# Performance work log

Hardware: AMD Instinct MI355X
Metric: run time of the kernel (lower is better)

The kernel has to match this reference:

```python
import jax, jax.numpy as jnp
import numpy as np

B, N, D, NH = 16, 512, 4096, 16
DK = D // NH  # 256; note N must equal 2*DK for the bias broadcast to be valid


def setup_inputs() -> dict:
    key = jax.random.key(0)
    ks = jax.random.split(key, 7)
    s = 1.0 / np.sqrt(D).astype(np.float32)
    return {
        "x": jax.random.normal(ks[0], (B, N, D), dtype=jnp.float32),
        "Augementation_embedding": jax.random.normal(ks[1], (B, N, D), dtype=jnp.float32),
        "Wq": jax.random.normal(ks[2], (D, D), dtype=jnp.float32) * s,
        "Wk": jax.random.normal(ks[3], (D, D), dtype=jnp.float32) * s,
        "Wv": jax.random.normal(ks[4], (D, D), dtype=jnp.float32) * s,
        "Wp": jax.random.normal(ks[5], (2 * D, D), dtype=jnp.float32) * s,
        "bp": jax.random.normal(ks[6], (2 * D,), dtype=jnp.float32) * 0.01,
    }


def reference(x, Augementation_embedding, Wq, Wk, Wv, Wp, bp):
    b, n, d = x.shape
    nh, dk = NH, DK
    scale = 1.0 / np.sqrt(dk)
    # torch nn.Linear computes x @ W.T
    q = (x @ Wq.T).reshape(b, n, nh, dk).transpose(0, 2, 1, 3)  # (b,nh,n,dk)
    k = (x @ Wk.T).reshape(b, n, nh, dk).transpose(0, 2, 1, 3)
    v = (x @ Wv.T).reshape(b, n, nh, dk).transpose(0, 2, 1, 3)
    # additive learned bias: (b,nh,n,2*dk) == (b,nh,n,n) since n == 2*dk
    ep = (Augementation_embedding @ Wp.T + bp).reshape(b, n, nh, 2 * dk).transpose(0, 2, 1, 3)
    dist = jnp.einsum("bhqd,bhkd->bhqk", q, k) * scale + ep  # (b,nh,n,n)
    dist = jax.nn.softmax(dist, axis=-1)
    att = jnp.einsum("bhqk,bhkd->bhqd", dist, v)  # (b,nh,n,dk)
    return att.transpose(0, 2, 1, 3).reshape(b, n, d)
```

## Files before the change

### kernel.cpp

```cpp
#include <hip/hip_runtime.h>
#include <hip/hip_bf16.h>

typedef __attribute__((ext_vector_type(4))) float f32x4;
typedef __attribute__((ext_vector_type(8))) short s16x8;
typedef __attribute__((ext_vector_type(4))) short s16x4;
typedef __attribute__((ext_vector_type(8))) unsigned short u16x8;
typedef __attribute__((ext_vector_type(4))) unsigned short u16x4;
typedef __attribute__((ext_vector_type(4))) float fv4;

#define DEV static __device__ __forceinline__

DEV unsigned short f2bf(float f) {
  union { float f; unsigned u; } v; v.f = f;
  return (unsigned short)((v.u + 0x7fffu + ((v.u >> 16) & 1u)) >> 16);
}
DEV float bf2f(unsigned short u) {
  union { unsigned u; float f; } v; v.u = ((unsigned)u) << 16; return v.f;
}

typedef const __attribute__((address_space(1))) void* gas_t;
typedef __attribute__((address_space(3))) void* las_t;
DEV void load_lds16(const void* g, void* l) {
  __builtin_amdgcn_global_load_lds((gas_t)g, (las_t)l, 16, 0, 0);
}

__global__ __launch_bounds__(256) void cvt_kernel(const float* __restrict__ in,
                                                  unsigned short* __restrict__ out,
                                                  int n4) {
  int i = blockIdx.x * 256 + threadIdx.x;
  int stride = gridDim.x * 256;
  for (; i < n4; i += stride) {
    fv4 v = *(const fv4*)(in + (size_t)i * 4);
    u16x4 o;
    o[0] = f2bf(v[0]); o[1] = f2bf(v[1]); o[2] = f2bf(v[2]); o[3] = f2bf(v[3]);
    *(u16x4*)(out + (size_t)i * 4) = o;
  }
}

template<int EPI>
__global__ __launch_bounds__(256, 2) void gemm128(const unsigned short* __restrict__ A,
                                                  const unsigned short* __restrict__ B,
                                                  unsigned short* __restrict__ C,
                                                  const float* __restrict__ bias,
                                                  int N, int K, int bxsh) {
  __shared__ unsigned short lds[3][12288];
  const int t = threadIdx.x;
  const int lane = t & 63;
  const int w = t >> 6;
  const int wr = w >> 1;
  const int wc = w & 1;
  const int r0 = lane & 15;
  const int g = lane >> 4;

  const int bid = blockIdx.x;
  const int bx = bid & ((1 << bxsh) - 1);
  const int by = bid >> bxsh;
  const long brow = (long)by * 128;
  const long bcol = (long)bx * 256;

  const int srow = t >> 2;
  const int scol = ((t & 3) ^ ((t >> 3) & 3)) * 8;
  const unsigned short* As = A + (brow + srow) * (long)K + scol;
  const unsigned short* Bs = B + (bcol + srow) * (long)K + scol;
  const int dst = t * 8;

#define STG(sl, kt)                                                  \
  do {                                                               \
    const long c0_ = (long)(kt) << 5;                                \
    load_lds16(As + c0_,                   &lds[sl][dst]);           \
    load_lds16(As + 64 * (long)K + c0_,    &lds[sl][2048 + dst]);    \
    load_lds16(Bs + c0_,                   &lds[sl][4096 + dst]);    \
    load_lds16(Bs + 64 * (long)K + c0_,    &lds[sl][6144 + dst]);    \
    load_lds16(Bs + 128 * (long)K + c0_,   &lds[sl][8192 + dst]);    \
    load_lds16(Bs + 192 * (long)K + c0_,   &lds[sl][10240 + dst]);   \
  } while (0)
#define SBAR __builtin_amdgcn_sched_barrier(0)

  f32x4 acc[4][8] = {};
  const int NT = K >> 5;

  const int cswz = (g ^ ((r0 >> 1) & 3)) * 8;
  const int arow = wr * 64 + r0;
  const int brw = wc * 128 + r0;

  if (bid & 1) __builtin_amdgcn_s_sleep(8);

  STG(0, 0);
  STG(1, 1);
  asm volatile("s_waitcnt vmcnt(6)" ::: "memory");
  __builtin_amdgcn_s_barrier();
  SBAR;

  int sl = 0;
  for (int kt = 0; kt < NT; ++kt) {
    int sl2 = sl + 2; if (sl2 >= 3) sl2 -= 3;
    if (kt + 2 < NT) STG(sl2, kt + 2);
    const unsigned short* Lp = &lds[sl][0];
    s16x8 AF[4], BF[8];
#pragma unroll
    for (int m = 0; m < 4; ++m)
      AF[m] = *(const s16x8*)&Lp[(arow + m * 16) * 32 + cswz];
#pragma unroll
    for (int n = 0; n < 8; ++n)
      BF[n] = *(const s16x8*)&Lp[4096 + (brw + n * 16) * 32 + cswz];
    SBAR;
    __builtin_amdgcn_s_setprio(1);
#pragma unroll
    for (int m = 0; m < 4; ++m)
#pragma unroll
      for (int n = 0; n < 8; ++n)
        acc[m][n] = __builtin_amdgcn_mfma_f32_16x16x32_bf16(AF[m], BF[n], acc[m][n], 0, 0, 0);
    __builtin_amdgcn_s_setprio(0);
    SBAR;
    if (kt + 2 < NT) asm volatile("s_waitcnt vmcnt(6)" ::: "memory");
    else             asm volatile("s_waitcnt vmcnt(0)" ::: "memory");
    __builtin_amdgcn_s_barrier();
    SBAR;
    sl = (sl == 2) ? 0 : sl + 1;
  }
#undef SBAR
#undef STG

  const int g4 = g * 4;
#pragma unroll
  for (int m = 0; m < 4; ++m) {
#pragma unroll
    for (int n = 0; n < 8; ++n) {
      f32x4 v = acc[m][n];
      long col = bcol + wc * 128 + n * 16 + r0;
#pragma unroll
      for (int r = 0; r < 4; ++r) {
        long row = brow + wr * 64 + m * 16 + g4 + r;
        float val = v[r];
        if (EPI == 1) val += bias[col];
        if (EPI == 2) {
          long addr = ((col >> 9) << 21) + (row << 9) + (col & 511);
          C[addr] = f2bf(val);
        } else {
          C[row * (long)N + col] = f2bf(val);
        }
      }
    }
  }
}

__global__ __launch_bounds__(512, 2) void attn_kernel(const unsigned short* __restrict__ Q,
                                                      const unsigned short* __restrict__ K,
                                                      const unsigned short* __restrict__ V,
                                                      const unsigned short* __restrict__ EP,
                                                      float* __restrict__ out) {
  __shared__ unsigned short lds[256 * 136];
  const int t = threadIdx.x;
  const int lane = t & 63;
  const int w = t >> 6;
  const int bid = blockIdx.x;
  const int qt = bid & 3;
  const int h = (bid >> 2) & 15;
  const int b = bid >> 6;
  const int r0 = lane & 15;
  const int g = lane >> 4;

  const int qrow = qt * 128 + w * 16;

  s16x8 qf[8];
  {
    const unsigned short* qp = Q + ((size_t)(b * 512 + qrow + r0)) * 4096 + h * 256 + g * 8;
#pragma unroll
    for (int s = 0; s < 8; ++s) qf[s] = *(const s16x8*)(qp + s * 32);
  }

  f32x4 st[32];
#pragma unroll
  for (int f = 0; f < 32; ++f) st[f] = f32x4{0.f, 0.f, 0.f, 0.f};

#pragma unroll
  for (int kc = 0; kc < 4; ++kc) {
    {
      const unsigned short* kp = K + ((size_t)(b * 512 + kc * 128)) * 4096 + h * 256;
#pragma unroll
      for (int u = 0; u < 8; ++u) {
        int fidx = u * 4096 + t * 8;
        int row = fidx >> 8, c = fidx & 255;
        u16x8 v = *(const u16x8*)(kp + (size_t)row * 4096 + c);
        *(u16x8*)&lds[row * 264 + c] = v;
      }
    }
    __syncthreads();
#pragma unroll
    for (int mf = 0; mf < 8; ++mf) {
      const unsigned short* lk = &lds[(mf * 16 + r0) * 264 + g * 8];
#pragma unroll
      for (int s = 0; s < 8; ++s) {
        s16x8 af = *(const s16x8*)(lk + s * 32);
        st[kc * 8 + mf] = __builtin_amdgcn_mfma_f32_16x16x32_bf16(af, qf[s], st[kc * 8 + mf], 0, 0, 0);
      }
    }
    __syncthreads();
  }

  {
    const unsigned short* ep = EP + ((size_t)(b * 512 + qrow + r0)) * 8192 + h * 512 + g * 4;
#pragma unroll
    for (int f = 0; f < 32; ++f) {
      u16x4 e = *(const u16x4*)(ep + f * 16);
#pragma unroll
      for (int r = 0; r < 4; ++r)
        st[f][r] = st[f][r] * 0.0625f + bf2f(e[r]);
    }
  }

  float mx = -1e30f;
#pragma unroll
  for (int f = 0; f < 32; ++f)
    mx = fmaxf(mx, fmaxf(fmaxf(st[f][0], st[f][1]), fmaxf(st[f][2], st[f][3])));
  mx = fmaxf(mx, __shfl_xor(mx, 16, 64));
  mx = fmaxf(mx, __shfl_xor(mx, 32, 64));
  float sum = 0.f;
#pragma unroll
  for (int f = 0; f < 32; ++f) {
#pragma unroll
    for (int r = 0; r < 4; ++r) {
      float e = __expf(st[f][r] - mx);
      st[f][r] = e;
      sum += e;
    }
  }
  sum += __shfl_xor(sum, 16, 64);
  sum += __shfl_xor(sum, 32, 64);
  const float rinv = 1.0f / sum;

  s16x8 pb[16];
#pragma unroll
  for (int p = 0; p < 16; ++p) {
    s16x8 v;
#pragma unroll
    for (int j = 0; j < 4; ++j) {
      v[j] = (short)f2bf(st[2 * p][j] * rinv);
      v[j + 4] = (short)f2bf(st[2 * p + 1][j] * rinv);
    }
    pb[p] = v;
  }

  f32x4 acc2[16];
#pragma unroll
  for (int d = 0; d < 16; ++d) acc2[d] = f32x4{0.f, 0.f, 0.f, 0.f};

#pragma unroll
  for (int kc = 0; kc < 4; ++kc) {
    {
      const unsigned short* vp = V + ((size_t)(b * 16 + h)) * 131072 + kc * 128;
#pragma unroll
      for (int u = 0; u < 8; ++u) {
        int fidx = u * 4096 + t * 8;
        int row = fidx >> 7, c = fidx & 127;
        u16x8 vv = *(const u16x8*)(vp + (size_t)row * 512 + c);
        *(u16x8*)&lds[row * 136 + c] = vv;
      }
    }
    __syncthreads();
#pragma unroll
    for (int d = 0; d < 16; ++d) {
      const unsigned short* lv = &lds[(d * 16 + r0) * 136 + g * 4];
#pragma unroll
      for (int p = 0; p < 4; ++p) {
        s16x4 a0 = *(const s16x4*)(lv + p * 32);
        s16x4 a1 = *(const s16x4*)(lv + p * 32 + 16);
        s16x8 av;
        av[0] = a0[0]; av[1] = a0[1]; av[2] = a0[2]; av[3] = a0[3];
        av[4] = a1[0]; av[5] = a1[1]; av[6] = a1[2]; av[7] = a1[3];
        acc2[d] = __builtin_amdgcn_mfma_f32_16x16x32_bf16(av, pb[kc * 4 + p], acc2[d], 0, 0, 0);
      }
    }
    __syncthreads();
  }

  {
    float* op = out + ((size_t)(b * 512 + qrow + r0)) * 4096 + h * 256 + g * 4;
#pragma unroll
    for (int d = 0; d < 16; ++d)
      *(fv4*)(op + d * 16) = acc2[d];
  }
}

extern "C" void kernel_launch(void* const* d_in, const int* in_sizes, int n_in,
                              void* d_out, int out_size, void* d_ws, size_t ws_size,
                              hipStream_t stream) {
  const float* x   = (const float*)d_in[0];
  const float* aug = (const float*)d_in[1];
  const float* wq  = (const float*)d_in[2];
  const float* wk  = (const float*)d_in[3];
  const float* wv  = (const float*)d_in[4];
  const float* wp  = (const float*)d_in[5];
  const float* bp  = (const float*)d_in[6];
  float* out = (float*)d_out;

  const size_t OFF_XA = 0;
  const size_t OFF_WQ = 67108864;
  const size_t OFF_WK = OFF_WQ + 33554432;
  const size_t OFF_WV = OFF_WK + 33554432;
  const size_t OFF_Q  = OFF_WQ + 100663296;
  const size_t OFF_K  = OFF_Q + 67108864;
  const size_t OFF_VT = OFF_K + 67108864;
  const size_t OFF_EP = OFF_VT + 67108864;
  const size_t NEED   = OFF_EP + 134217728;
  if (ws_size < NEED) return;

  char* ws = (char*)d_ws;
  unsigned short* x_bf   = (unsigned short*)(ws + OFF_XA);
  unsigned short* aug_bf = (unsigned short*)(ws + OFF_XA);
  unsigned short* wq_bf  = (unsigned short*)(ws + OFF_WQ);
  unsigned short* wk_bf  = (unsigned short*)(ws + OFF_WK);
  unsigned short* wv_bf  = (unsigned short*)(ws + OFF_WV);
  unsigned short* wp_bf  = (unsigned short*)(ws + OFF_WQ);
  unsigned short* q_bf   = (unsigned short*)(ws + OFF_Q);
  unsigned short* k_bf   = (unsigned short*)(ws + OFF_K);
  unsigned short* vt_bf  = (unsigned short*)(ws + OFF_VT);
  unsigned short* ep_bf  = (unsigned short*)(ws + OFF_EP);

  cvt_kernel<<<2048, 256, 0, stream>>>(x, x_bf, 33554432 / 4);
  cvt_kernel<<<2048, 256, 0, stream>>>(wq, wq_bf, 16777216 / 4);
  cvt_kernel<<<2048, 256, 0, stream>>>(wk, wk_bf, 16777216 / 4);
  cvt_kernel<<<2048, 256, 0, stream>>>(wv, wv_bf, 16777216 / 4);

  gemm128<0><<<1024, 256, 0, stream>>>(x_bf, wq_bf, q_bf, nullptr, 4096, 4096, 4);
  gemm128<0><<<1024, 256, 0, stream>>>(x_bf, wk_bf, k_bf, nullptr, 4096, 4096, 4);
  gemm128<2><<<1024, 256, 0, stream>>>(wv_bf, x_bf, vt_bf, nullptr, 8192, 4096, 5);

  cvt_kernel<<<2048, 256, 0, stream>>>(aug, aug_bf, 33554432 / 4);
  cvt_kernel<<<2048, 256, 0, stream>>>(wp, wp_bf, 33554432 / 4);
  gemm128<1><<<2048, 256, 0, stream>>>(aug_bf, wp_bf, ep_bf, bp, 8192, 4096, 5);

  attn_kernel<<<1024, 512, 0, stream>>>(q_bf, k_bf, vt_bf, ep_bf, out);
}
```

Before: 1.767 ms.

## Replace per-iteration workgroup barrier with LDS flag polling between waves

The GEMM main loop swaps its per-k-step s_barrier for LDS-resident per-wave progress counters that each wave polls: one counter records that a stage's global-to-LDS loads have landed, the other records that its LDS fragment reads are done. Waves can then drift apart within the triple-buffer window instead of lock-stepping every iteration. The odd-block start sleep is removed. The cost is spin-polling with s_sleep, extra LDS traffic and waitcnts, and a risk of memory-ordering bugs, since global_load_lds completion seen by one wave is not obviously visible to others without a barrier.

```diff
diff --git a/kernel.cpp b/kernel.cpp
--- a/kernel.cpp
+++ b/kernel.cpp
@@ -44,6 +44,9 @@
                                                   const float* __restrict__ bias,
                                                   int N, int K, int bxsh) {
   __shared__ unsigned short lds[3][12288];
+  __shared__ int flags[8];
+  volatile int* vfl = flags;
+
   const int t = threadIdx.x;
   const int lane = t & 63;
   const int w = t >> 6;
@@ -74,7 +77,18 @@
     load_lds16(Bs + 128 * (long)K + c0_,   &lds[sl][8192 + dst]);    \
     load_lds16(Bs + 192 * (long)K + c0_,   &lds[sl][10240 + dst]);   \
   } while (0)
-#define SBAR __builtin_amdgcn_sched_barrier(0)
+
+#define POLL_GE(base, target)                                        \
+  do {                                                               \
+    for (;;) {                                                       \
+      int m0_ = vfl[(base) + 0]; int m1_ = vfl[(base) + 1];          \
+      int m2_ = vfl[(base) + 2]; int m3_ = vfl[(base) + 3];          \
+      int mm_ = min(min(m0_, m1_), min(m2_, m3_));                   \
+      if (mm_ >= (target)) break;                                    \
+      __builtin_amdgcn_s_sleep(1);                                   \
+    }                                                                \
+    asm volatile("" ::: "memory");                                   \
+  } while (0)
 
   f32x4 acc[4][8] = {};
   const int NT = K >> 5;
@@ -83,18 +97,26 @@
   const int arow = wr * 64 + r0;
   const int brw = wc * 128 + r0;
 
-  if (bid & 1) __builtin_amdgcn_s_sleep(8);
-
+  if (lane == 0) { vfl[w] = -1; vfl[4 + w] = -1; }
   STG(0, 0);
   STG(1, 1);
   asm volatile("s_waitcnt vmcnt(6)" ::: "memory");
-  __builtin_amdgcn_s_barrier();
-  SBAR;
+  if (lane == 0) vfl[w] = 0;
+  __syncthreads();
 
   int sl = 0;
   for (int kt = 0; kt < NT; ++kt) {
+    POLL_GE(4, kt - 1);
     int sl2 = sl + 2; if (sl2 >= 3) sl2 -= 3;
-    if (kt + 2 < NT) STG(sl2, kt + 2);
+    if (kt + 2 < NT) {
+      STG(sl2, kt + 2);
+      asm volatile("s_waitcnt vmcnt(6)" ::: "memory");
+      if (lane == 0) vfl[w] = kt + 1;
+    } else if (kt == NT - 2) {
+      asm volatile("s_waitcnt vmcnt(0)" ::: "memory");
+      if (lane == 0) vfl[w] = NT - 1;
+    }
+    POLL_GE(0, kt);
     const unsigned short* Lp = &lds[sl][0];
     s16x8 AF[4], BF[8];
 #pragma unroll
@@ -103,7 +125,9 @@
 #pragma unroll
     for (int n = 0; n < 8; ++n)
       BF[n] = *(const s16x8*)&Lp[4096 + (brw + n * 16) * 32 + cswz];
-    SBAR;
+    asm volatile("s_waitcnt lgkmcnt(0)" ::: "memory");
+    __builtin_amdgcn_sched_barrier(0);
+    if (lane == 0) vfl[4 + w] = kt;
     __builtin_amdgcn_s_setprio(1);
 #pragma unroll
     for (int m = 0; m < 4; ++m)
@@ -111,14 +135,10 @@
       for (int n = 0; n < 8; ++n)
         acc[m][n] = __builtin_amdgcn_mfma_f32_16x16x32_bf16(AF[m], BF[n], acc[m][n], 0, 0, 0);
     __builtin_amdgcn_s_setprio(0);
-    SBAR;
-    if (kt + 2 < NT) asm volatile("s_waitcnt vmcnt(6)" ::: "memory");
-    else             asm volatile("s_waitcnt vmcnt(0)" ::: "memory");
-    __builtin_amdgcn_s_barrier();
-    SBAR;
+    __builtin_amdgcn_sched_barrier(0);
     sl = (sl == 2) ? 0 : sl + 1;
   }
-#undef SBAR
+#undef POLL_GE
 #undef STG
 
   const int g4 = g * 4;
```

Result: slower. 1.994 ms (+12.9%).
